# Optimization experiments

Hardware: AMD Instinct MI355X
Metric: run time of the kernel (lower is better)

## Reference

```python
import jax, jax.numpy as jnp
import numpy as np

B, D, CL, QL = 32, 128, 1024, 512


def setup_inputs() -> dict:
    key = jax.random.key(0)
    kC, kQ, kW = jax.random.split(key, 3)
    C = jax.random.normal(kC, (B, D, CL), dtype=jnp.float32)
    Q = jax.random.normal(kQ, (B, D, QL), dtype=jnp.float32)
    # xavier_normal_ on (B*CL, 1, 3D): std = sqrt(2 / (fan_in + fan_out)) = sqrt(2/(1+3D))
    std = (2.0 / (1.0 + 3.0 * D)) ** 0.5
    W = jax.random.normal(kW, (B * CL, 1, 3 * D), dtype=jnp.float32) * std
    return {"C": C, "Q": Q, "W": W}


def reference(C, Q, W):
    # C: (B, D, CL), Q: (B, D, QL), W: (B*CL, 1, 3D)
    b, d, cl = C.shape
    Ct = jnp.transpose(C, (0, 2, 1))   # (B, CL, D)
    Qt = jnp.transpose(Q, (0, 2, 1))   # (B, QL, D)
    Wr = W.reshape(b, cl, 3 * d)
    wq, wc, wqc = Wr[..., :d], Wr[..., d:2 * d], Wr[..., 2 * d:]
    # Trilinear similarity: S[b,c,q] = wq[b,c].Q[b,q] + wc[b,c].C[b,c] + wqc[b,c].(C[b,c]*Q[b,q])
    S = (jnp.einsum('bcd,bqd->bcq', wq, Qt)
         + jnp.sum(wc * Ct, axis=-1, keepdims=True)
         + jnp.einsum('bcd,bqd->bcq', wqc * Ct, Qt))   # (B, CL, QL)
    S1 = jax.nn.softmax(S, axis=2)  # over queries
    S2 = jax.nn.softmax(S, axis=1)  # over context
    A = jnp.einsum('bcq,bqd->bcd', S1, Qt)             # (B, CL, D)
    # B = (S1 @ S2^T) @ C, reassociated as S1 @ (S2^T @ C) to avoid (CL,CL) intermediate
    S2tC = jnp.einsum('bkq,bkd->bqd', S2, Ct)          # (B, QL, D)
    Bm = jnp.einsum('bcq,bqd->bcd', S1, S2tC)          # (B, CL, D)
    out = jnp.concatenate([Ct, A, Ct * A, Ct * Bm], axis=2)  # (B, CL, 4D)
    # dropout is identity in eval mode
    return jnp.transpose(out, (0, 2, 1))               # (B, 4D, CL)
```

## Files before the change

### kernel.cpp

```cpp
#include <hip/hip_runtime.h>
#include <hip/hip_bf16.h>
#include <cstddef>

#define B_  32
#define D_  128
#define CL_ 1024
#define QL_ 512

using short8  = __attribute__((ext_vector_type(8))) short;
using short4v = __attribute__((ext_vector_type(4))) short;
using float4v = __attribute__((ext_vector_type(4))) float;

__device__ __forceinline__ unsigned short f2bf(float f) {
    unsigned int u = __float_as_uint(f);
    u += 0x7FFFu + ((u >> 16) & 1u);
    return (unsigned short)(u >> 16);
}
__device__ __forceinline__ float bf2f(unsigned short h) {
    return __uint_as_float(((unsigned int)h) << 16);
}

__device__ __forceinline__ void swz_bt(int i, int& b, int& t) {
    b = (i & 7) + 8 * (i >> 7);
    t = (i >> 3) & 15;
}

__global__ __launch_bounds__(256) void k_u_bias(const float* __restrict__ C,
                                                const float* __restrict__ W,
                                                unsigned short* __restrict__ U,
                                                float* __restrict__ bias,
                                                unsigned short* __restrict__ Cbf) {
    int b  = blockIdx.y;
    int c0 = blockIdx.x * 32;
    int tid = threadIdx.x;

    __shared__ float tile[128][33];
    __shared__ float bred[32][9];

    for (int pass = 0; pass < 16; ++pass) {
        int d = pass * 8 + (tid >> 5);
        int c = tid & 31;
        float v = C[((size_t)(b * D_ + d)) * CL_ + c0 + c];
        tile[d][c] = v;
        Cbf[((size_t)(b * D_ + d)) * CL_ + c0 + c] = f2bf(v);
    }
    __syncthreads();

    int tc    = tid >> 3;
    int lane8 = tid & 7;
    int c     = c0 + tc;
    size_t wbase = ((size_t)(b * CL_ + c)) * (3 * D_);
    size_t ubase = ((size_t)(b * CL_ + c)) * D_;

    float bpart = 0.f;
    #pragma unroll
    for (int i = 0; i < 4; ++i) {
        int d = i * 32 + lane8 * 4;
        float4 wq4  = *(const float4*)(W + wbase + d);
        float4 wc4  = *(const float4*)(W + wbase + D_ + d);
        float4 wqc4 = *(const float4*)(W + wbase + 2 * D_ + d);
        float ct0 = tile[d + 0][tc], ct1 = tile[d + 1][tc];
        float ct2 = tile[d + 2][tc], ct3 = tile[d + 3][tc];
        short4v u;
        u[0] = (short)f2bf(wq4.x + wqc4.x * ct0);
        u[1] = (short)f2bf(wq4.y + wqc4.y * ct1);
        u[2] = (short)f2bf(wq4.z + wqc4.z * ct2);
        u[3] = (short)f2bf(wq4.w + wqc4.w * ct3);
        *(short4v*)(U + ubase + d) = u;
        bpart += wc4.x * ct0 + wc4.y * ct1 + wc4.z * ct2 + wc4.w * ct3;
    }
    bred[tc][lane8] = bpart;
    __syncthreads();
    if (lane8 == 0) {
        float s = 0.f;
        for (int i = 0; i < 8; ++i) s += bred[tc][i];
        bias[b * CL_ + c] = s;
    }
}

__global__ __launch_bounds__(256) void k_qt(const float* __restrict__ Q,
                                            unsigned short* __restrict__ Qt,
                                            unsigned short* __restrict__ Qbf) {
    int b  = blockIdx.z;
    int d0 = blockIdx.y * 64;
    int q0 = blockIdx.x * 64;
    int tid = threadIdx.x;
    __shared__ float t[64][65];
    for (int p = 0; p < 16; ++p) {
        int d = p * 4 + (tid >> 6);
        int q = tid & 63;
        float v = Q[((size_t)(b * D_ + d0 + d)) * QL_ + q0 + q];
        t[d][q] = v;
        Qbf[((size_t)(b * D_ + d0 + d)) * QL_ + q0 + q] = f2bf(v);
    }
    __syncthreads();
    for (int p = 0; p < 16; ++p) {
        int q  = p * 4 + (tid >> 6);
        int dd = tid & 63;
        Qt[((size_t)(b * QL_ + q0 + q)) * D_ + d0 + dd] = f2bf(t[dd][q]);
    }
}

__global__ __launch_bounds__(256) void k_gs2(const unsigned short* __restrict__ Ubf,
                                             const unsigned short* __restrict__ Qtbf,
                                             const float* __restrict__ bias,
                                             unsigned short* __restrict__ Sbf,
                                             float* __restrict__ rmax,
                                             float* __restrict__ rinv,
                                             float* __restrict__ pcmax,
                                             float* __restrict__ pcsum) {
    int b, mt;
    swz_bt(blockIdx.x, b, mt);
    int m0 = mt * 64;
    int tid  = threadIdx.x;
    int lane = tid & 63, wave = tid >> 6;
    int wm = wave >> 1, wn = wave & 1;
    int quad = lane >> 4, l15 = lane & 15;

    __shared__ __align__(16) short As[64][136];
    __shared__ __align__(16) short Bs[64][136];
    __shared__ float sbias[64];
    __shared__ float rmw[2][64], rsw[2][64];
    __shared__ float cmw[2][64], csw[2][64];

    const unsigned short* Ab = Ubf  + ((size_t)(b * CL_ + m0)) * D_;
    const unsigned short* Bb = Qtbf + ((size_t)(b * QL_)) * D_;

    #pragma unroll
    for (int i = 0; i < 4; ++i) {
        int flat = tid + i * 256;
        int row = flat >> 4, col = (flat & 15) * 8;
        *(short8*)&As[row][col] = *(const short8*)(Ab + (size_t)row * D_ + col);
    }
    if (tid < 64) sbias[tid] = bias[b * CL_ + m0 + tid];

    float rm_run[2][4], rs_run[2][4];
    #pragma unroll
    for (int fi = 0; fi < 2; ++fi)
        #pragma unroll
        for (int rr = 0; rr < 4; ++rr) { rm_run[fi][rr] = -1e30f; rs_run[fi][rr] = 0.f; }

    for (int chunk = 0; chunk < 8; ++chunk) {
        __syncthreads();
        #pragma unroll
        for (int i = 0; i < 4; ++i) {
            int flat = tid + i * 256;
            int row = flat >> 4, col = (flat & 15) * 8;
            *(short8*)&Bs[row][col] = *(const short8*)(Bb + (size_t)(chunk * 64 + row) * D_ + col);
        }
        __syncthreads();

        float4v acc[2][2] = {};
        #pragma unroll
        for (int ks = 0; ks < 128; ks += 32) {
            short8 af0 = *(const short8*)&As[wm * 32 + l15][ks + quad * 8];
            short8 af1 = *(const short8*)&As[wm * 32 + 16 + l15][ks + quad * 8];
            short8 bf0 = *(const short8*)&Bs[wn * 32 + l15][ks + quad * 8];
            short8 bf1 = *(const short8*)&Bs[wn * 32 + 16 + l15][ks + quad * 8];
            acc[0][0] = __builtin_amdgcn_mfma_f32_16x16x32_bf16(af0, bf0, acc[0][0], 0, 0, 0);
            acc[0][1] = __builtin_amdgcn_mfma_f32_16x16x32_bf16(af0, bf1, acc[0][1], 0, 0, 0);
            acc[1][0] = __builtin_amdgcn_mfma_f32_16x16x32_bf16(af1, bf0, acc[1][0], 0, 0, 0);
            acc[1][1] = __builtin_amdgcn_mfma_f32_16x16x32_bf16(af1, bf1, acc[1][1], 0, 0, 0);
        }

        float v[2][2][4];
        #pragma unroll
        for (int fi = 0; fi < 2; ++fi)
            #pragma unroll
            for (int fj = 0; fj < 2; ++fj)
                #pragma unroll
                for (int rr = 0; rr < 4; ++rr) {
                    int mloc = wm * 32 + fi * 16 + quad * 4 + rr;
                    float x = acc[fi][fj][rr] + sbias[mloc];
                    v[fi][fj][rr] = x;
                    int nloc = wn * 32 + fj * 16 + l15;
                    Sbf[((size_t)(b * CL_ + m0 + mloc)) * QL_ + chunk * 64 + nloc] = f2bf(x);
                }

        #pragma unroll
        for (int fi = 0; fi < 2; ++fi)
            #pragma unroll
            for (int rr = 0; rr < 4; ++rr) {
                float v0 = v[fi][0][rr], v1 = v[fi][1][rr];
                float nm = fmaxf(rm_run[fi][rr], fmaxf(v0, v1));
                rs_run[fi][rr] = rs_run[fi][rr] * __expf(rm_run[fi][rr] - nm)
                               + __expf(v0 - nm) + __expf(v1 - nm);
                rm_run[fi][rr] = nm;
            }

        #pragma unroll
        for (int fj = 0; fj < 2; ++fj) {
            float cm = v[0][fj][0];
            #pragma unroll
            for (int fi = 0; fi < 2; ++fi)
                #pragma unroll
                for (int rr = 0; rr < 4; ++rr) cm = fmaxf(cm, v[fi][fj][rr]);
            float cs = 0.f;
            #pragma unroll
            for (int fi = 0; fi < 2; ++fi)
                #pragma unroll
                for (int rr = 0; rr < 4; ++rr) cs += __expf(v[fi][fj][rr] - cm);
            #pragma unroll
            for (int off = 16; off <= 32; off <<= 1) {
                float om = __shfl_xor(cm, off);
                float os = __shfl_xor(cs, off);
                float nm = fmaxf(cm, om);
                cs = cs * __expf(cm - nm) + os * __expf(om - nm);
                cm = nm;
            }
            if (quad == 0) {
                int col = wn * 32 + fj * 16 + l15;
                cmw[wm][col] = cm;
                csw[wm][col] = cs;
            }
        }
        __syncthreads();
        if (tid < 64) {
            float m0v = cmw[0][tid], s0v = csw[0][tid];
            float m1v = cmw[1][tid], s1v = csw[1][tid];
            float nm = fmaxf(m0v, m1v);
            float ss = s0v * __expf(m0v - nm) + s1v * __expf(m1v - nm);
            size_t pi = ((size_t)(b * 16 + mt)) * QL_ + chunk * 64 + tid;
            pcmax[pi] = nm;
            pcsum[pi] = ss;
        }
    }

    #pragma unroll
    for (int off = 1; off <= 8; off <<= 1)
        #pragma unroll
        for (int fi = 0; fi < 2; ++fi)
            #pragma unroll
            for (int rr = 0; rr < 4; ++rr) {
                float om = __shfl_xor(rm_run[fi][rr], off);
                float os = __shfl_xor(rs_run[fi][rr], off);
                float nm = fmaxf(rm_run[fi][rr], om);
                rs_run[fi][rr] = rs_run[fi][rr] * __expf(rm_run[fi][rr] - nm)
                               + os * __expf(om - nm);
                rm_run[fi][rr] = nm;
            }
    if (l15 == 0) {
        #pragma unroll
        for (int fi = 0; fi < 2; ++fi)
            #pragma unroll
            for (int rr = 0; rr < 4; ++rr) {
                int m = wm * 32 + fi * 16 + quad * 4 + rr;
                rmw[wn][m] = rm_run[fi][rr];
                rsw[wn][m] = rs_run[fi][rr];
            }
    }
    __syncthreads();
    if (tid < 64) {
        float m0v = rmw[0][tid], s0v = rsw[0][tid];
        float m1v = rmw[1][tid], s1v = rsw[1][tid];
        float nm = fmaxf(m0v, m1v);
        float ss = s0v * __expf(m0v - nm) + s1v * __expf(m1v - nm);
        rmax[b * CL_ + m0 + tid] = nm;
        rinv[b * CL_ + m0 + tid] = 1.0f / ss;
    }
}

__global__ __launch_bounds__(256) void k_gp(const unsigned short* __restrict__ Cbf,
                                            const unsigned short* __restrict__ Sbf,
                                            const float* __restrict__ pcmax,
                                            const float* __restrict__ pcsum,
                                            unsigned short* __restrict__ Pbf) {
    int b, qt;
    swz_bt(blockIdx.x, b, qt);
    int q0 = qt * 32;

    int tid  = threadIdx.x;
    int lane = tid & 63, wave = tid >> 6;
    int quad = lane >> 4, l15 = lane & 15;

    __shared__ __align__(16) short As[128][72];
    __shared__ __align__(16) short Bs[32][72];
    __shared__ float scm[32], sci[32];

    if (tid < 32) {
        float M = -1e30f, SS = 0.f;
        #pragma unroll
        for (int ch = 0; ch < 16; ++ch) {
            size_t idx = ((size_t)(b * 16 + ch)) * QL_ + q0 + tid;
            float m = pcmax[idx], s = pcsum[idx];
            float nM = fmaxf(M, m);
            SS = SS * __expf(M - nM) + s * __expf(m - nM);
            M = nM;
        }
        scm[tid] = M;
        sci[tid] = 1.0f / SS;
    }
    __syncthreads();

    const unsigned short* Cb = Cbf + (size_t)b * D_ * CL_;
    const unsigned short* Sb = Sbf + (size_t)b * CL_ * QL_;

    int arow = tid >> 3;
    int acol = (tid & 7) * 8;
    int srow = tid >> 4;
    int uq   = tid & 15;

    float4v acc[2][2] = {};

    for (int k0 = 0; k0 < CL_; k0 += 64) {
        #pragma unroll
        for (int p = 0; p < 4; ++p) {
            int row = p * 32 + arow;
            *(short8*)&As[row][acol] = *(const short8*)(Cb + (size_t)row * CL_ + k0 + acol);
        }
        #pragma unroll
        for (int p = 0; p < 4; ++p) {
            int crow = p * 16 + srow;
            unsigned int raw = *(const unsigned int*)(Sb + (size_t)(k0 + crow) * QL_ + q0 + 2 * uq);
            float v0 = __expf(bf2f((unsigned short)(raw & 0xFFFF)) - scm[2 * uq]) * sci[2 * uq];
            float v1 = __expf(bf2f((unsigned short)(raw >> 16)) - scm[2 * uq + 1]) * sci[2 * uq + 1];
            Bs[2 * uq][crow]     = (short)f2bf(v0);
            Bs[2 * uq + 1][crow] = (short)f2bf(v1);
        }
        __syncthreads();
        #pragma unroll
        for (int ks = 0; ks < 64; ks += 32) {
            short8 a0 = *(const short8*)&As[wave * 32 + l15][ks + quad * 8];
            short8 a1 = *(const short8*)&As[wave * 32 + 16 + l15][ks + quad * 8];
            short8 b0 = *(const short8*)&Bs[l15][ks + quad * 8];
            short8 b1 = *(const short8*)&Bs[16 + l15][ks + quad * 8];
            acc[0][0] = __builtin_amdgcn_mfma_f32_16x16x32_bf16(a0, b0, acc[0][0], 0, 0, 0);
            acc[0][1] = __builtin_amdgcn_mfma_f32_16x16x32_bf16(a0, b1, acc[0][1], 0, 0, 0);
            acc[1][0] = __builtin_amdgcn_mfma_f32_16x16x32_bf16(a1, b0, acc[1][0], 0, 0, 0);
            acc[1][1] = __builtin_amdgcn_mfma_f32_16x16x32_bf16(a1, b1, acc[1][1], 0, 0, 0);
        }
        __syncthreads();
    }

    #pragma unroll
    for (int fi = 0; fi < 2; ++fi)
        #pragma unroll
        for (int fj = 0; fj < 2; ++fj)
            #pragma unroll
            for (int rr = 0; rr < 4; ++rr) {
                int d = wave * 32 + fi * 16 + quad * 4 + rr;
                int q = q0 + fj * 16 + l15;
                Pbf[((size_t)(b * D_ + d)) * QL_ + q] = f2bf(acc[fi][fj][rr]);
            }
}

__global__ __launch_bounds__(256) void k_av2(const unsigned short* __restrict__ Qbf,
                                             const unsigned short* __restrict__ Pbf,
                                             const unsigned short* __restrict__ Sbf,
                                             const float* __restrict__ rmax,
                                             const float* __restrict__ rinv,
                                             const float* __restrict__ C,
                                             float* __restrict__ out) {
    int b, nt;
    swz_bt(blockIdx.x, b, nt);
    int n0 = nt * 64;

    int tid  = threadIdx.x;
    int lane = tid & 63, wave = tid >> 6;
    int wm = wave >> 1, wn = wave & 1;
    int quad = lane >> 4, l15 = lane & 15;

    __shared__ __align__(16) short AsQ[128][72];
    __shared__ __align__(16) short AsP[128][72];
    __shared__ __align__(16) short Bs[64][72];
    __shared__ float srm[64], sri[64];

    if (tid < 64) {
        srm[tid] = rmax[b * CL_ + n0 + tid];
        sri[tid] = rinv[b * CL_ + n0 + tid];
    }
    __syncthreads();

    const unsigned short* Qb = Qbf + (size_t)b * D_ * QL_;
    const unsigned short* Pb = Pbf + (size_t)b * D_ * QL_;
    const unsigned short* Sb = Sbf + ((size_t)(b * CL_ + n0)) * QL_;

    int arow = tid >> 3;
    int acol = (tid & 7) * 8;
    int brow = tid >> 2;
    int bcol = (tid & 3) * 16;
    float brm = srm[brow], bri = sri[brow];

    float4v accQ[4][2] = {};
    float4v accP[4][2] = {};

    for (int k0 = 0; k0 < QL_; k0 += 64) {
        #pragma unroll
        for (int p = 0; p < 4; ++p) {
            int row = p * 32 + arow;
            *(short8*)&AsQ[row][acol] = *(const short8*)(Qb + (size_t)row * QL_ + k0 + acol);
            *(short8*)&AsP[row][acol] = *(const short8*)(Pb + (size_t)row * QL_ + k0 + acol);
        }
        #pragma unroll
        for (int h = 0; h < 2; ++h) {
            uint4 raw = *(const uint4*)(Sb + (size_t)brow * QL_ + k0 + bcol + h * 8);
            unsigned int rw[4] = {raw.x, raw.y, raw.z, raw.w};
            short8 vv;
            #pragma unroll
            for (int j = 0; j < 8; ++j) {
                unsigned short bits = (unsigned short)((rw[j >> 1] >> ((j & 1) * 16)) & 0xFFFF);
                vv[j] = (short)f2bf(__expf(bf2f(bits) - brm) * bri);
            }
            *(short8*)&Bs[brow][bcol + h * 8] = vv;
        }
        __syncthreads();
        #pragma unroll
        for (int ks = 0; ks < 64; ks += 32) {
            short8 b0 = *(const short8*)&Bs[wn * 32 + l15][ks + quad * 8];
            short8 b1 = *(const short8*)&Bs[wn * 32 + 16 + l15][ks + quad * 8];
            #pragma unroll
            for (int fi = 0; fi < 4; ++fi) {
                short8 aq = *(const short8*)&AsQ[wm * 64 + fi * 16 + l15][ks + quad * 8];
                accQ[fi][0] = __builtin_amdgcn_mfma_f32_16x16x32_bf16(aq, b0, accQ[fi][0], 0, 0, 0);
                accQ[fi][1] = __builtin_amdgcn_mfma_f32_16x16x32_bf16(aq, b1, accQ[fi][1], 0, 0, 0);
            }
            #pragma unroll
            for (int fi = 0; fi < 4; ++fi) {
                short8 ap = *(const short8*)&AsP[wm * 64 + fi * 16 + l15][ks + quad * 8];
                accP[fi][0] = __builtin_amdgcn_mfma_f32_16x16x32_bf16(ap, b0, accP[fi][0], 0, 0, 0);
                accP[fi][1] = __builtin_amdgcn_mfma_f32_16x16x32_bf16(ap, b1, accP[fi][1], 0, 0, 0);
            }
        }
        __syncthreads();
    }

    #pragma unroll
    for (int fi = 0; fi < 4; ++fi)
        #pragma unroll
        for (int fj = 0; fj < 2; ++fj)
            #pragma unroll
            for (int rr = 0; rr < 4; ++rr) {
                int d = wm * 64 + fi * 16 + quad * 4 + rr;
                int c = n0 + wn * 32 + fj * 16 + l15;
                float ct = C[((size_t)(b * D_ + d)) * CL_ + c];
                float vq = accQ[fi][fj][rr];
                float vp = accP[fi][fj][rr];
                size_t ob = ((size_t)(b * 4 * D_ + d)) * CL_ + c;
                out[ob]                        = ct;
                out[ob + (size_t)D_ * CL_]     = vq;
                out[ob + 2 * (size_t)D_ * CL_] = ct * vq;
                out[ob + 3 * (size_t)D_ * CL_] = ct * vp;
            }
}

extern "C" void kernel_launch(void* const* d_in, const int* in_sizes, int n_in,
                              void* d_out, int out_size, void* d_ws, size_t ws_size,
                              hipStream_t stream) {
    const float* C = (const float*)d_in[0];
    const float* Q = (const float*)d_in[1];
    const float* W = (const float*)d_in[2];
    float* out = (float*)d_out;

    unsigned short* Ubf  = (unsigned short*)d_ws;
    unsigned short* Qtbf = Ubf  + (size_t)B_ * CL_ * D_;
    unsigned short* Qbf  = Qtbf + (size_t)B_ * QL_ * D_;
    unsigned short* Cbf  = Qbf  + (size_t)B_ * D_ * QL_;
    unsigned short* Pbf  = Cbf  + (size_t)B_ * D_ * CL_;
    unsigned short* Sbf  = Pbf  + (size_t)B_ * D_ * QL_;
    float* bias  = (float*)(Sbf + (size_t)B_ * CL_ * QL_);
    float* rmax  = bias  + (size_t)B_ * CL_;
    float* rinv  = rmax  + (size_t)B_ * CL_;
    float* pcmax = rinv  + (size_t)B_ * CL_;
    float* pcsum = pcmax + (size_t)B_ * 16 * QL_;

    k_u_bias<<<dim3(CL_ / 32, B_), 256, 0, stream>>>(C, W, Ubf, bias, Cbf);
    k_qt<<<dim3(QL_ / 64, D_ / 64, B_), 256, 0, stream>>>(Q, Qtbf, Qbf);
    k_gs2<<<512, 256, 0, stream>>>(Ubf, Qtbf, bias, Sbf, rmax, rinv, pcmax, pcsum);
    k_gp<<<512, 256, 0, stream>>>(Cbf, Sbf, pcmax, pcsum, Pbf);
    k_av2<<<512, 256, 0, stream>>>(Qbf, Pbf, Sbf, rmax, rinv, C, out);
}
```

Measured before the change: 195.4 us.

## Software-pipeline global loads with register prefetch and LDS double buffering across kernels

```diff
diff --git a/kernel.cpp b/kernel.cpp
--- a/kernel.cpp
+++ b/kernel.cpp
@@ -118,10 +118,10 @@
     int quad = lane >> 4, l15 = lane & 15;
 
     __shared__ __align__(16) short As[64][136];
-    __shared__ __align__(16) short Bs[64][136];
+    __shared__ __align__(16) short Bs[2][64][136];
     __shared__ float sbias[64];
     __shared__ float rmw[2][64], rsw[2][64];
-    __shared__ float cmw[2][64], csw[2][64];
+    __shared__ float cmw[2][8][64], csw[2][8][64];
 
     const unsigned short* Ab = Ubf  + ((size_t)(b * CL_ + m0)) * D_;
     const unsigned short* Bb = Qtbf + ((size_t)(b * QL_)) * D_;
@@ -130,7 +130,8 @@
     for (int i = 0; i < 4; ++i) {
         int flat = tid + i * 256;
         int row = flat >> 4, col = (flat & 15) * 8;
-        *(short8*)&As[row][col] = *(const short8*)(Ab + (size_t)row * D_ + col);
+        *(short8*)&As[row][col]    = *(const short8*)(Ab + (size_t)row * D_ + col);
+        *(short8*)&Bs[0][row][col] = *(const short8*)(Bb + (size_t)row * D_ + col);
     }
     if (tid < 64) sbias[tid] = bias[b * CL_ + m0 + tid];
 
@@ -140,13 +141,16 @@
         #pragma unroll
         for (int rr = 0; rr < 4; ++rr) { rm_run[fi][rr] = -1e30f; rs_run[fi][rr] = 0.f; }
 
+    short8 pre[4];
     for (int chunk = 0; chunk < 8; ++chunk) {
-        __syncthreads();
-        #pragma unroll
-        for (int i = 0; i < 4; ++i) {
-            int flat = tid + i * 256;
-            int row = flat >> 4, col = (flat & 15) * 8;
-            *(short8*)&Bs[row][col] = *(const short8*)(Bb + (size_t)(chunk * 64 + row) * D_ + col);
+        int cur = chunk & 1;
+        if (chunk < 7) {
+            #pragma unroll
+            for (int i = 0; i < 4; ++i) {
+                int flat = tid + i * 256;
+                int row = flat >> 4, col = (flat & 15) * 8;
+                pre[i] = *(const short8*)(Bb + (size_t)((chunk + 1) * 64 + row) * D_ + col);
+            }
         }
         __syncthreads();
 
@@ -155,8 +159,8 @@
         for (int ks = 0; ks < 128; ks += 32) {
             short8 af0 = *(const short8*)&As[wm * 32 + l15][ks + quad * 8];
             short8 af1 = *(const short8*)&As[wm * 32 + 16 + l15][ks + quad * 8];
-            short8 bf0 = *(const short8*)&Bs[wn * 32 + l15][ks + quad * 8];
-            short8 bf1 = *(const short8*)&Bs[wn * 32 + 16 + l15][ks + quad * 8];
+            short8 bf0 = *(const short8*)&Bs[cur][wn * 32 + l15][ks + quad * 8];
+            short8 bf1 = *(const short8*)&Bs[cur][wn * 32 + 16 + l15][ks + quad * 8];
             acc[0][0] = __builtin_amdgcn_mfma_f32_16x16x32_bf16(af0, bf0, acc[0][0], 0, 0, 0);
             acc[0][1] = __builtin_amdgcn_mfma_f32_16x16x32_bf16(af0, bf1, acc[0][1], 0, 0, 0);
             acc[1][0] = __builtin_amdgcn_mfma_f32_16x16x32_bf16(af1, bf0, acc[1][0], 0, 0, 0);
@@ -210,20 +214,32 @@
             }
             if (quad == 0) {
                 int col = wn * 32 + fj * 16 + l15;
-                cmw[wm][col] = cm;
-                csw[wm][col] = cs;
-            }
-        }
-        __syncthreads();
-        if (tid < 64) {
-            float m0v = cmw[0][tid], s0v = csw[0][tid];
-            float m1v = cmw[1][tid], s1v = csw[1][tid];
-            float nm = fmaxf(m0v, m1v);
-            float ss = s0v * __expf(m0v - nm) + s1v * __expf(m1v - nm);
-            size_t pi = ((size_t)(b * 16 + mt)) * QL_ + chunk * 64 + tid;
-            pcmax[pi] = nm;
-            pcsum[pi] = ss;
-        }
+                cmw[wm][chunk][col] = cm;
+                csw[wm][chunk][col] = cs;
+            }
+        }
+
+        if (chunk < 7) {
+            #pragma unroll
+            for (int i = 0; i < 4; ++i) {
+                int flat = tid + i * 256;
+                int row = flat >> 4, col = (flat & 15) * 8;
+                *(short8*)&Bs[cur ^ 1][row][col] = pre[i];
+            }
+        }
+    }
+    __syncthreads();
+
+    #pragma unroll
+    for (int e = 0; e < 2; ++e) {
+        int idx = tid + e * 256;
+        int ch = idx >> 6, col = idx & 63;
+        float m0v = cmw[0][ch][col], m1v = cmw[1][ch][col];
+        float nm = fmaxf(m0v, m1v);
+        float ss = csw[0][ch][col] * __expf(m0v - nm) + csw[1][ch][col] * __expf(m1v - nm);
+        size_t pi = ((size_t)(b * 16 + mt)) * QL_ + ch * 64 + col;
+        pcmax[pi] = nm;
+        pcsum[pi] = ss;
     }
 
     #pragma unroll
@@ -273,9 +289,27 @@
     int lane = tid & 63, wave = tid >> 6;
     int quad = lane >> 4, l15 = lane & 15;
 
-    __shared__ __align__(16) short As[128][72];
-    __shared__ __align__(16) short Bs[32][72];
+    __shared__ __align__(16) short As[2][128][72];
+    __shared__ __align__(16) short Bs[2][32][72];
     __shared__ float scm[32], sci[32];
+
+    const unsigned short* Cb = Cbf + (size_t)b * D_ * CL_;
+    const unsigned short* Sb = Sbf + (size_t)b * CL_ * QL_;
+
+    int arow = tid >> 3;
+    int acol = (tid & 7) * 8;
+    int srow = tid >> 4;
+    int uq   = tid & 15;
+
+    short8 apre[4];
+    unsigned int spre[4];
+
+    #pragma unroll
+    for (int p = 0; p < 4; ++p)
+        apre[p] = *(const short8*)(Cb + (size_t)(p * 32 + arow) * CL_ + acol);
+    #pragma unroll
+    for (int p = 0; p < 4; ++p)
+        spre[p] = *(const unsigned int*)(Sb + (size_t)(p * 16 + srow) * QL_ + q0 + 2 * uq);
 
     if (tid < 32) {
         float M = -1e30f, SS = 0.f;
@@ -292,44 +326,60 @@
     }
     __syncthreads();
 
-    const unsigned short* Cb = Cbf + (size_t)b * D_ * CL_;
-    const unsigned short* Sb = Sbf + (size_t)b * CL_ * QL_;
-
-    int arow = tid >> 3;
-    int acol = (tid & 7) * 8;
-    int srow = tid >> 4;
-    int uq   = tid & 15;
+    #pragma unroll
+    for (int p = 0; p < 4; ++p)
+        *(short8*)&As[0][p * 32 + arow][acol] = apre[p];
+    #pragma unroll
+    for (int p = 0; p < 4; ++p) {
+        int crow = p * 16 + srow;
+        unsigned int raw = spre[p];
+        float v0 = __expf(bf2f((unsigned short)(raw & 0xFFFF)) - scm[2 * uq]) * sci[2 * uq];
+        float v1 = __expf(bf2f((unsigned short)(raw >> 16)) - scm[2 * uq + 1]) * sci[2 * uq + 1];
+        Bs[0][2 * uq][crow]     = (short)f2bf(v0);
+        Bs[0][2 * uq + 1][crow] = (short)f2bf(v1);
+    }
 
     float4v acc[2][2] = {};
 
-    for (int k0 = 0; k0 < CL_; k0 += 64) {
-        #pragma unroll
-        for (int p = 0; p < 4; ++p) {
-            int row = p * 32 + arow;
-            *(short8*)&As[row][acol] = *(const short8*)(Cb + (size_t)row * CL_ + k0 + acol);
-        }
-        #pragma unroll
-        for (int p = 0; p < 4; ++p) {
-            int crow = p * 16 + srow;
-            unsigned int raw = *(const unsigned int*)(Sb + (size_t)(k0 + crow) * QL_ + q0 + 2 * uq);
-            float v0 = __expf(bf2f((unsigned short)(raw & 0xFFFF)) - scm[2 * uq]) * sci[2 * uq];
-            float v1 = __expf(bf2f((unsigned short)(raw >> 16)) - scm[2 * uq + 1]) * sci[2 * uq + 1];
-            Bs[2 * uq][crow]     = (short)f2bf(v0);
-            Bs[2 * uq + 1][crow] = (short)f2bf(v1);
+    for (int step = 0; step < 16; ++step) {
+        int cur = step & 1;
+        int k0n = (step + 1) * 64;
+        if (step < 15) {
+            #pragma unroll
+            for (int p = 0; p < 4; ++p)
+                apre[p] = *(const short8*)(Cb + (size_t)(p * 32 + arow) * CL_ + k0n + acol);
+            #pragma unroll
+            for (int p = 0; p < 4; ++p)
+                spre[p] = *(const unsigned int*)(Sb + (size_t)(k0n + p * 16 + srow) * QL_ + q0 + 2 * uq);
         }
         __syncthreads();
+
         #pragma unroll
         for (int ks = 0; ks < 64; ks += 32) {
-            short8 a0 = *(const short8*)&As[wave * 32 + l15][ks + quad * 8];
-            short8 a1 = *(const short8*)&As[wave * 32 + 16 + l15][ks + quad * 8];
-            short8 b0 = *(const short8*)&Bs[l15][ks + quad * 8];
-            short8 b1 = *(const short8*)&Bs[16 + l15][ks + quad * 8];
+            short8 a0 = *(const short8*)&As[cur][wave * 32 + l15][ks + quad * 8];
+            short8 a1 = *(const short8*)&As[cur][wave * 32 + 16 + l15][ks + quad * 8];
+            short8 b0 = *(const short8*)&Bs[cur][l15][ks + quad * 8];
+            short8 b1 = *(const short8*)&Bs[cur][16 + l15][ks + quad * 8];
             acc[0][0] = __builtin_amdgcn_mfma_f32_16x16x32_bf16(a0, b0, acc[0][0], 0, 0, 0);
             acc[0][1] = __builtin_amdgcn_mfma_f32_16x16x32_bf16(a0, b1, acc[0][1], 0, 0, 0);
             acc[1][0] = __builtin_amdgcn_mfma_f32_16x16x32_bf16(a1, b0, acc[1][0], 0, 0, 0);
             acc[1][1] = __builtin_amdgcn_mfma_f32_16x16x32_bf16(a1, b1, acc[1][1], 0, 0, 0);
         }
-        __syncthreads();
+
+        if (step < 15) {
+            #pragma unroll
+            for (int p = 0; p < 4; ++p)
+                *(short8*)&As[cur ^ 1][p * 32 + arow][acol] = apre[p];
+            #pragma unroll
+            for (int p = 0; p < 4; ++p) {
+                int crow = p * 16 + srow;
+                unsigned int raw = spre[p];
+                float v0 = __expf(bf2f((unsigned short)(raw & 0xFFFF)) - scm[2 * uq]) * sci[2 * uq];
+                float v1 = __expf(bf2f((unsigned short)(raw >> 16)) - scm[2 * uq + 1]) * sci[2 * uq + 1];
+                Bs[cur ^ 1][2 * uq][crow]     = (short)f2bf(v0);
+                Bs[cur ^ 1][2 * uq + 1][crow] = (short)f2bf(v1);
+            }
+        }
     }
 
     #pragma unroll
@@ -369,7 +419,6 @@
         srm[tid] = rmax[b * CL_ + n0 + tid];
         sri[tid] = rinv[b * CL_ + n0 + tid];
     }
-    __syncthreads();
 
     const unsigned short* Qb = Qbf + (size_t)b * D_ * QL_;
     const unsigned short* Pb = Pbf + (size_t)b * D_ * QL_;
@@ -379,6 +428,20 @@
     int acol = (tid & 7) * 8;
     int brow = tid >> 2;
     int bcol = (tid & 3) * 16;
+
+    short8 qa[4], pa[4];
+    uint4 sraw[2];
+    #pragma unroll
+    for (int p = 0; p < 4; ++p) {
+        int row = p * 32 + arow;
+        qa[p] = *(const short8*)(Qb + (size_t)row * QL_ + acol);
+        pa[p] = *(const short8*)(Pb + (size_t)row * QL_ + acol);
+    }
+    #pragma unroll
+    for (int h = 0; h < 2; ++h)
+        sraw[h] = *(const uint4*)(Sb + (size_t)brow * QL_ + bcol + h * 8);
+
+    __syncthreads();
     float brm = srm[brow], bri = sri[brow];
 
     float4v accQ[4][2] = {};
@@ -388,13 +451,12 @@
         #pragma unroll
         for (int p = 0; p < 4; ++p) {
             int row = p * 32 + arow;
-            *(short8*)&AsQ[row][acol] = *(const short8*)(Qb + (size_t)row * QL_ + k0 + acol);
-            *(short8*)&AsP[row][acol] = *(const short8*)(Pb + (size_t)row * QL_ + k0 + acol);
+            *(short8*)&AsQ[row][acol] = qa[p];
+            *(short8*)&AsP[row][acol] = pa[p];
         }
         #pragma unroll
         for (int h = 0; h < 2; ++h) {
-            uint4 raw = *(const uint4*)(Sb + (size_t)brow * QL_ + k0 + bcol + h * 8);
-            unsigned int rw[4] = {raw.x, raw.y, raw.z, raw.w};
+            unsigned int rw[4] = {sraw[h].x, sraw[h].y, sraw[h].z, sraw[h].w};
             short8 vv;
             #pragma unroll
             for (int j = 0; j < 8; ++j) {
@@ -404,6 +466,19 @@
             *(short8*)&Bs[brow][bcol + h * 8] = vv;
         }
         __syncthreads();
+
+        if (k0 + 64 < QL_) {
+            #pragma unroll
+            for (int p = 0; p < 4; ++p) {
+                int row = p * 32 + arow;
+                qa[p] = *(const short8*)(Qb + (size_t)row * QL_ + k0 + 64 + acol);
+                pa[p] = *(const short8*)(Pb + (size_t)row * QL_ + k0 + 64 + acol);
+            }
+            #pragma unroll
+            for (int h = 0; h < 2; ++h)
+                sraw[h] = *(const uint4*)(Sb + (size_t)brow * QL_ + k0 + 64 + bcol + h * 8);
+        }
+
         #pragma unroll
         for (int ks = 0; ks < 64; ks += 32) {
             short8 b0 = *(const short8*)&Bs[wn * 32 + l15][ks + quad * 8];
```

New measurement: 188.9 us (median of 2 runs). 1.03x faster.
